# Performance work log

Measured on AMD Instinct MI355X. Metric: run time of the kernel, lower is better.

The kernel has to match this reference:

```python
import jax, jax.numpy as jnp
import numpy as np

N = 100000
E = 1600000
D_IN = 256
N_HEADS = 4
OUT_SZ = 32  # output_dim // n_heads = 128 // 4
ALPHA = 0.2  # leaky relu slope


def setup_inputs() -> dict:
    key = jax.random.key(0)
    ks = jax.random.split(key, 8)
    x = jax.random.normal(ks[0], (N, D_IN), dtype=jnp.float32)
    edge_row = jax.random.randint(ks[1], (E,), 0, N, dtype=jnp.int32)
    edge_col = jax.random.randint(ks[2], (E,), 0, N, dtype=jnp.int32)
    # per-head params: W (conv1d k=1, no bias), a1/a2 (conv1d k=1 with bias)
    W = jax.random.normal(ks[3], (N_HEADS, D_IN, OUT_SZ), dtype=jnp.float32) * (1.0 / np.sqrt(D_IN))
    a1 = jax.random.normal(ks[4], (N_HEADS, OUT_SZ), dtype=jnp.float32) * (1.0 / np.sqrt(OUT_SZ))
    b1 = jnp.zeros((N_HEADS,), dtype=jnp.float32)
    a2 = jax.random.normal(ks[5], (N_HEADS, OUT_SZ), dtype=jnp.float32) * (1.0 / np.sqrt(OUT_SZ))
    b2 = jnp.zeros((N_HEADS,), dtype=jnp.float32)
    return {"x": x, "W": W, "a1": a1, "b1": b1, "a2": a2, "b2": b2,
            "edge_row": edge_row, "edge_col": edge_col}


def _gat_heads(x, W, a1, b1, a2, b2, edge_row, edge_col):
    # per-head linear transform: [H, N, O]
    fts = jnp.einsum('nd,hdo->hno', x, W)
    f1 = jnp.einsum('hno,ho->hn', fts, a1) + b1[:, None]  # [H, N]
    f2 = jnp.einsum('hno,ho->hn', fts, a2) + b2[:, None]  # [H, N]
    # edge logits: f1[row] + f2[col]  (adj values are 1)
    logits = f1[:, edge_row] + f2[:, edge_col]            # [H, E]
    lr = jnp.maximum(ALPHA * logits, logits)
    # segment softmax over each node's incoming edge set (rows)
    seg_max = jax.vmap(lambda v: jax.ops.segment_max(v, edge_row, num_segments=N))(lr)
    ex = jnp.exp(lr - seg_max[:, edge_row])
    denom = jax.vmap(lambda v: jax.ops.segment_sum(v, edge_row, num_segments=N))(ex)
    coef = ex / denom[:, edge_row]                        # [H, E]
    # SpMM aggregation: out[h, i] = sum_{e: row(e)=i} coef[h,e] * fts[h, col(e)]
    msg = coef[:, :, None] * fts[:, edge_col, :]          # [H, E, O]
    agg = jax.vmap(lambda m: jax.ops.segment_sum(m, edge_row, num_segments=N))(msg)  # [H, N, O]
    h = jnp.transpose(agg, (1, 0, 2)).reshape(N, N_HEADS * OUT_SZ)  # concat heads
    return jax.nn.elu(h)[None]  # [1, N, output_dim]


def reference(x, W, a1, b1, a2, b2, edge_row, edge_col):
    return _gat_heads(x, W, a1, b1, a2, b2, edge_row, edge_col)
```

## Files before the change

kernel.cpp:

```cpp
#include <hip/hip_runtime.h>
#include <hip/hip_bf16.h>
#include <math.h>

#define ALPHA 0.2f
#define PB_EDGES 4096

typedef __attribute__((ext_vector_type(8))) short short8;
typedef __attribute__((ext_vector_type(4))) float floatx4;

__device__ __forceinline__ ushort f2bf(float f) {
    uint u = __float_as_uint(f);
    u += 0x7fff + ((u >> 16) & 1);
    return (ushort)(u >> 16);
}

__device__ __forceinline__ short8 pack8(float4 lo, float4 hi) {
    short8 r;
    r[0] = (short)f2bf(lo.x); r[1] = (short)f2bf(lo.y);
    r[2] = (short)f2bf(lo.z); r[3] = (short)f2bf(lo.w);
    r[4] = (short)f2bf(hi.x); r[5] = (short)f2bf(hi.y);
    r[6] = (short)f2bf(hi.z); r[7] = (short)f2bf(hi.w);
    return r;
}

__global__ __launch_bounds__(256) void k_wprep(const float* __restrict__ W,
                                               ushort* __restrict__ Wt)
{
    int g = blockIdx.x * 256 + threadIdx.x;
    int c = g >> 8, d = g & 255;
    Wt[g] = f2bf(W[(c >> 5) * 8192 + d * 32 + (c & 31)]);
}

__global__ __launch_bounds__(256) void k_gemm(const float* __restrict__ x,
                                              const ushort* __restrict__ Wt,
                                              const float* __restrict__ a1v,
                                              const float* __restrict__ b1v,
                                              const float* __restrict__ a2v,
                                              const float* __restrict__ b2v,
                                              ushort* __restrict__ fts2,
                                              float* __restrict__ f1,
                                              float* __restrict__ f2, int M)
{
    __shared__ __align__(16) ushort smem[32768];
    const int t  = threadIdx.x;
    const int m0 = blockIdx.x * 128;

#pragma unroll
    for (int i = 0; i < 16; i++) {
        int f = i * 256 + t;
        int lane_ = f & 63, ksct = f >> 6;
        int ks = ksct & 7, ct = ksct >> 3;
        int mm = lane_ & 15, qq = lane_ >> 4;
        *(uint4*)&smem[f * 8] = *(const uint4*)&Wt[(ct * 16 + mm) * 256 + ks * 32 + qq * 8];
    }

    const int w = t >> 6, lane = t & 63;
    const int mm = lane & 15, qq = lane >> 4;

    int row0 = m0 + w * 32 + mm;
    int row1 = row0 + 16;
    int r0c = (row0 < M) ? row0 : (M - 1);
    int r1c = (row1 < M) ? row1 : (M - 1);
    const float* ar0 = x + (size_t)r0c * 256 + qq * 8;
    const float* ar1 = x + (size_t)r1c * 256 + qq * 8;
    short8 afrag[2][8];
#pragma unroll
    for (int ks = 0; ks < 8; ks++) {
        float4 lo0 = *(const float4*)(ar0 + ks * 32);
        float4 hi0 = *(const float4*)(ar0 + ks * 32 + 4);
        float4 lo1 = *(const float4*)(ar1 + ks * 32);
        float4 hi1 = *(const float4*)(ar1 + ks * 32 + 4);
        afrag[0][ks] = pack8(lo0, hi0);
        afrag[1][ks] = pack8(lo1, hi1);
    }

    floatx4 acc[2][8];
#pragma unroll
    for (int r = 0; r < 2; r++)
#pragma unroll
        for (int ct = 0; ct < 8; ct++) acc[r][ct] = (floatx4){0.f, 0.f, 0.f, 0.f};

    __syncthreads();

#pragma unroll
    for (int ks = 0; ks < 8; ks++) {
#pragma unroll
        for (int ct = 0; ct < 8; ct++) {
            short8 b8 = *(const short8*)&smem[((ct * 8 + ks) * 64 + lane) * 8];
            acc[0][ct] = __builtin_amdgcn_mfma_f32_16x16x32_bf16(afrag[0][ks], b8, acc[0][ct], 0, 0, 0);
            acc[1][ct] = __builtin_amdgcn_mfma_f32_16x16x32_bf16(afrag[1][ks], b8, acc[1][ct], 0, 0, 0);
        }
    }

    __syncthreads();
    ushort* ftsL = smem;
#pragma unroll
    for (int r = 0; r < 2; r++)
#pragma unroll
        for (int ct = 0; ct < 8; ct++)
#pragma unroll
            for (int i = 0; i < 4; i++) {
                int rowl = w * 32 + r * 16 + qq * 4 + i;
                ftsL[rowl * 136 + ct * 16 + mm] = f2bf(acc[r][ct][i]);
            }
    __syncthreads();

    {
        int rowl = t >> 1, half = t & 1;
        int gr = m0 + rowl;
        if (gr < M) {
            const uint4* src = (const uint4*)&ftsL[rowl * 136 + half * 64];
            uint4* dst = (uint4*)(fts2 + (size_t)gr * 128 + half * 64);
#pragma unroll
            for (int i = 0; i < 8; i++) dst[i] = src[i];
        }
    }
#pragma unroll
    for (int p = 0; p < 2; p++) {
        int task = p * 256 + t;
        int rowl = task >> 2, h = task & 3;
        int gr = m0 + rowl;
        if (gr < M) {
            const ushort* fr = &ftsL[rowl * 136 + h * 32];
            float s1 = 0.f, s2 = 0.f;
#pragma unroll
            for (int o = 0; o < 32; o++) {
                float v = __uint_as_float((uint)fr[o] << 16);
                s1 = fmaf(v, a1v[h * 32 + o], s1);
                s2 = fmaf(v, a2v[h * 32 + o], s2);
            }
            f1[gr * 4 + h] = s1 + b1v[h];
            f2[gr * 4 + h] = s2 + b2v[h];
        }
    }
}

__global__ __launch_bounds__(256) void k_phist(const int* __restrict__ erow,
                                               int* __restrict__ bcnt, int E, int NB)
{
    __shared__ int h[512];
    for (int i = threadIdx.x; i < 512; i += 256) h[i] = 0;
    __syncthreads();
    int b0 = blockIdx.x * PB_EDGES;
    int bend = b0 + PB_EDGES; if (bend > E) bend = E;
    for (int j = b0 + threadIdx.x; j < bend; j += 256)
        atomicAdd(&h[erow[j] >> 8], 1);
    __syncthreads();
    for (int i = threadIdx.x; i < NB; i += 256)
        if (h[i]) atomicAdd(&bcnt[i], h[i]);
}

__global__ __launch_bounds__(256) void k_scan_buckets(const int* __restrict__ bcnt,
                                                      int* __restrict__ base,
                                                      int* __restrict__ bcursor,
                                                      int NB, int E)
{
    __shared__ int s[256];
    int t = threadIdx.x;
    int i0 = 2 * t, i1 = 2 * t + 1;
    int v0 = (i0 < NB) ? bcnt[i0] : 0;
    int v1 = (i1 < NB) ? bcnt[i1] : 0;
    int tsum = v0 + v1;
    s[t] = tsum;
    __syncthreads();
    for (int off = 1; off < 256; off <<= 1) {
        int u = (t >= off) ? s[t - off] : 0;
        __syncthreads();
        s[t] += u;
        __syncthreads();
    }
    int excl = s[t] - tsum;
    if (i0 < NB) { base[i0] = excl;      bcursor[i0] = excl; }
    if (i1 < NB) { base[i1] = excl + v0; bcursor[i1] = excl + v0; }
    if (t == 0) base[NB] = E;
}

__global__ __launch_bounds__(256) void k_pscatter(const int* __restrict__ erow,
                                                  const int* __restrict__ ecol,
                                                  int* __restrict__ bcursor,
                                                  uint* __restrict__ part, int E)
{
    __shared__ int h[512];
    __shared__ int cur[512];
    for (int i = threadIdx.x; i < 512; i += 256) h[i] = 0;
    __syncthreads();
    int b0 = blockIdx.x * PB_EDGES;
    int bend = b0 + PB_EDGES; if (bend > E) bend = E;
    for (int j = b0 + threadIdx.x; j < bend; j += 256)
        atomicAdd(&h[erow[j] >> 8], 1);
    __syncthreads();
    for (int i = threadIdx.x; i < 512; i += 256)
        cur[i] = h[i] ? atomicAdd(&bcursor[i], h[i]) : 0;
    __syncthreads();
    for (int j = b0 + threadIdx.x; j < bend; j += 256) {
        int r = erow[j], c = ecol[j];
        int p = atomicAdd(&cur[r >> 8], 1);
        part[p] = ((uint)(r & 255) << 24) | (uint)c;
    }
}

__global__ __launch_bounds__(256) void k_bucket(const uint* __restrict__ part,
                                                const int* __restrict__ base,
                                                int* __restrict__ row_start,
                                                int* __restrict__ col_sorted,
                                                int Nn, int NB, int E)
{
    __shared__ int cnt[256];
    __shared__ int s[256];
    __shared__ int cur[256];
    const int b = blockIdx.x, t = threadIdx.x;
    const int start = base[b], end = base[b + 1];

    cnt[t] = 0;
    __syncthreads();
    for (int j = start + t; j < end; j += 256)
        atomicAdd(&cnt[part[j] >> 24], 1);
    __syncthreads();
    int v = cnt[t];
    s[t] = v;
    __syncthreads();
    for (int off = 1; off < 256; off <<= 1) {
        int u = (t >= off) ? s[t - off] : 0;
        __syncthreads();
        s[t] += u;
        __syncthreads();
    }
    int excl = s[t] - v;
    int r = b * 256 + t;
    if (r < Nn) row_start[r] = start + excl;
    if (b == 0 && t == 0) row_start[Nn] = E;
    cur[t] = start + excl;
    __syncthreads();
    for (int j = start + t; j < end; j += 256) {
        uint rc = part[j];
        int p = atomicAdd(&cur[rc >> 24], 1);
        col_sorted[p] = (int)(rc & 0xffffffu);
    }
}

__global__ __launch_bounds__(256) void k_gat_row(const ushort* __restrict__ fts2,
                                                 const float4* __restrict__ f1,
                                                 const float4* __restrict__ f2,
                                                 const int* __restrict__ row_start,
                                                 const int* __restrict__ cols,
                                                 float* __restrict__ out, int Nn)
{
    __shared__ float eL[4][256];
    __shared__ int   cL[4][64];

    const int wid  = threadIdx.x >> 6;
    const int lane = threadIdx.x & 63;
    const int r = blockIdx.x * 4 + wid;
    if (r >= Nn) return;

    const int s = row_start[r], e = row_start[r + 1];
    const int hl = lane >> 4;

    float2* outp = (float2*)(out + (size_t)r * 128);
    if (s == e) { outp[lane] = make_float2(0.f, 0.f); return; }

    const float4 f1r = f1[r];
    float ds0 = 0.f, ds1 = 0.f, ds2 = 0.f, ds3 = 0.f;
    float acc0 = 0.f, acc1 = 0.f;

    for (int j0 = s; j0 < e; j0 += 64) {
        int j = j0 + lane;
        bool act = (j < e);
        int c = act ? cols[j] : 0;
        float4 f2v = f2[c];
        float l0 = f1r.x + f2v.x; l0 = fmaxf(l0, ALPHA * l0);
        float l1 = f1r.y + f2v.y; l1 = fmaxf(l1, ALPHA * l1);
        float l2 = f1r.z + f2v.z; l2 = fmaxf(l2, ALPHA * l2);
        float l3 = f1r.w + f2v.w; l3 = fmaxf(l3, ALPHA * l3);
        float e0 = act ? __expf(l0) : 0.f;
        float e1 = act ? __expf(l1) : 0.f;
        float e2 = act ? __expf(l2) : 0.f;
        float e3 = act ? __expf(l3) : 0.f;
        ds0 += e0; ds1 += e1; ds2 += e2; ds3 += e3;

        asm volatile("s_waitcnt lgkmcnt(0)" ::: "memory");
        ((float4*)eL[wid])[lane] = make_float4(e0, e1, e2, e3);
        cL[wid][lane] = c;
        asm volatile("s_waitcnt lgkmcnt(0)" ::: "memory");

        int len = e - j0; if (len > 64) len = 64;
#pragma unroll 4
        for (int jj = 0; jj < len; jj++) {
            float ee = eL[wid][jj * 4 + hl];
            int   cc = cL[wid][jj];
            const uint* fp = (const uint*)(fts2 + (size_t)cc * 128);
            uint vv = fp[lane];
            float vx = __uint_as_float(vv << 16);
            float vy = __uint_as_float(vv & 0xffff0000u);
            acc0 = fmaf(ee, vx, acc0);
            acc1 = fmaf(ee, vy, acc1);
        }
    }

#pragma unroll
    for (int off = 32; off > 0; off >>= 1) {
        ds0 += __shfl_xor(ds0, off, 64);
        ds1 += __shfl_xor(ds1, off, 64);
        ds2 += __shfl_xor(ds2, off, 64);
        ds3 += __shfl_xor(ds3, off, 64);
    }
    float dsel = (hl == 0) ? ds0 : (hl == 1) ? ds1 : (hl == 2) ? ds2 : ds3;

    float o0 = acc0 / dsel;
    float o1 = acc1 / dsel;
    o0 = (o0 > 0.f) ? o0 : (__expf(o0) - 1.0f);
    o1 = (o1 > 0.f) ? o1 : (__expf(o1) - 1.0f);
    outp[lane] = make_float2(o0, o1);
}

extern "C" void kernel_launch(void* const* d_in, const int* in_sizes, int n_in,
                              void* d_out, int out_size, void* d_ws, size_t ws_size,
                              hipStream_t stream)
{
    const float* x   = (const float*)d_in[0];
    const float* W   = (const float*)d_in[1];
    const float* a1  = (const float*)d_in[2];
    const float* b1  = (const float*)d_in[3];
    const float* a2  = (const float*)d_in[4];
    const float* b2  = (const float*)d_in[5];
    const int*   erow = (const int*)d_in[6];
    const int*   ecol = (const int*)d_in[7];
    float* out = (float*)d_out;

    const int N = in_sizes[0] / 256;
    const int E = in_sizes[6];
    const int NB = (N + 255) >> 8;

    char*  ws  = (char*)d_ws;
    size_t off = 0;
    auto carve = [&](size_t bytes) -> char* {
        char* p = ws + off;
        off += (bytes + 255) & ~(size_t)255;
        return p;
    };
    ushort* fts2      = (ushort*)carve((size_t)N * 128 * 2);
    ushort* Wt        = (ushort*)carve((size_t)128 * 256 * 2);
    float*  f1        = (float*)carve((size_t)N * 4 * 4);
    float*  f2        = (float*)carve((size_t)N * 4 * 4);
    int*    row_start = (int*)carve(((size_t)N + 1) * 4);
    int*    bcnt      = (int*)carve(512 * 4);
    int*    base      = (int*)carve(513 * 4);
    int*    bcursor   = (int*)carve(512 * 4);
    int*    col_sorted= (int*)carve((size_t)E * 4);
    uint*   part      = (uint*)carve((size_t)E * 4);
    (void)ws_size;

    k_wprep<<<128, 256, 0, stream>>>(W, Wt);
    k_gemm<<<(N + 127) / 128, 256, 0, stream>>>(x, Wt, a1, b1, a2, b2, fts2, f1, f2, N);

    hipMemsetAsync(bcnt, 0, 512 * 4, stream);
    int npb = (E + PB_EDGES - 1) / PB_EDGES;
    k_phist<<<npb, 256, 0, stream>>>(erow, bcnt, E, NB);
    k_scan_buckets<<<1, 256, 0, stream>>>(bcnt, base, bcursor, NB, E);
    k_pscatter<<<npb, 256, 0, stream>>>(erow, ecol, bcursor, part, E);
    k_bucket<<<NB, 256, 0, stream>>>(part, base, row_start, col_sorted, N, NB, E);

    k_gat_row<<<(N + 3) / 4, 256, 0, stream>>>(fts2, (const float4*)f1, (const float4*)f2,
                                               row_start, col_sorted, out, N);
}
```

Baseline: 340.7 us.

## Process four edges per wave iteration with 16-byte gathers in GAT aggregation

The aggregation loop now splits each 64-lane wave into four 16-lane slots. Each slot handles a different edge, and each lane loads 16 bytes (8 bf16 values) of the neighbor feature row instead of 4 bytes. Column indices are stored pre-shifted as byte offsets to save address math. Partial accumulators are combined across slots with cross-lane shuffles at the end, and only slot 0 writes the output. The intent is fewer loop iterations and wider memory transactions for the gather, at the cost of more registers and an extra reduction.

Result: no change. 341.9 us (+0.4%).

```diff
diff --git a/kernel.cpp b/kernel.cpp
--- a/kernel.cpp
+++ b/kernel.cpp
@@ -245,8 +245,8 @@
                                                  const int* __restrict__ cols,
                                                  float* __restrict__ out, int Nn)
 {
-    __shared__ float eL[4][256];
-    __shared__ int   cL[4][64];
+    __shared__ __align__(16) float eL[4][256];
+    __shared__ uint vL[4][64];
 
     const int wid  = threadIdx.x >> 6;
     const int lane = threadIdx.x & 63;
@@ -254,14 +254,30 @@
     if (r >= Nn) return;
 
     const int s = row_start[r], e = row_start[r + 1];
-    const int hl = lane >> 4;
-
-    float2* outp = (float2*)(out + (size_t)r * 128);
-    if (s == e) { outp[lane] = make_float2(0.f, 0.f); return; }
+
+    const int slot = lane >> 4;
+    const int sub  = lane & 15;
+    const int hsel = sub >> 2;
+
+    float4* dst = (float4*)(out + (size_t)r * 128 + sub * 8);
+    if (s == e) {
+        if (slot == 0) {
+            dst[0] = make_float4(0.f, 0.f, 0.f, 0.f);
+            dst[1] = make_float4(0.f, 0.f, 0.f, 0.f);
+        }
+        return;
+    }
 
     const float4 f1r = f1[r];
     float ds0 = 0.f, ds1 = 0.f, ds2 = 0.f, ds3 = 0.f;
-    float acc0 = 0.f, acc1 = 0.f;
+    float acc[8];
+#pragma unroll
+    for (int i = 0; i < 8; i++) acc[i] = 0.f;
+
+    const float* eBase   = &eL[wid][slot * 4 + hsel];
+    const uint*  vBase   = &vL[wid][slot];
+    const char*  ftsB    = (const char*)fts2;
+    const uint   laneOff = (uint)sub * 16;
 
     for (int j0 = s; j0 < e; j0 += 64) {
         int j = j0 + lane;
@@ -280,23 +296,33 @@
 
         asm volatile("s_waitcnt lgkmcnt(0)" ::: "memory");
         ((float4*)eL[wid])[lane] = make_float4(e0, e1, e2, e3);
-        cL[wid][lane] = c;
+        vL[wid][lane] = (uint)c << 8;
         asm volatile("s_waitcnt lgkmcnt(0)" ::: "memory");
 
         int len = e - j0; if (len > 64) len = 64;
+        int ng = (len + 3) >> 2;
 #pragma unroll 4
-        for (int jj = 0; jj < len; jj++) {
-            float ee = eL[wid][jj * 4 + hl];
-            int   cc = cL[wid][jj];
-            const uint* fp = (const uint*)(fts2 + (size_t)cc * 128);
-            uint vv = fp[lane];
-            float vx = __uint_as_float(vv << 16);
-            float vy = __uint_as_float(vv & 0xffff0000u);
-            acc0 = fmaf(ee, vx, acc0);
-            acc1 = fmaf(ee, vy, acc1);
-        }
-    }
-
+        for (int g = 0; g < ng; g++) {
+            float ee = eBase[g * 16];
+            uint  vo = vBase[g * 4] + laneOff;
+            uint4 vv = *(const uint4*)(ftsB + vo);
+            float ve;
+            ve = __uint_as_float(vv.x << 16);          acc[0] = fmaf(ee, ve, acc[0]);
+            ve = __uint_as_float(vv.x & 0xffff0000u);  acc[1] = fmaf(ee, ve, acc[1]);
+            ve = __uint_as_float(vv.y << 16);          acc[2] = fmaf(ee, ve, acc[2]);
+            ve = __uint_as_float(vv.y & 0xffff0000u);  acc[3] = fmaf(ee, ve, acc[3]);
+            ve = __uint_as_float(vv.z << 16);          acc[4] = fmaf(ee, ve, acc[4]);
+            ve = __uint_as_float(vv.z & 0xffff0000u);  acc[5] = fmaf(ee, ve, acc[5]);
+            ve = __uint_as_float(vv.w << 16);          acc[6] = fmaf(ee, ve, acc[6]);
+            ve = __uint_as_float(vv.w & 0xffff0000u);  acc[7] = fmaf(ee, ve, acc[7]);
+        }
+    }
+
+#pragma unroll
+    for (int i = 0; i < 8; i++) {
+        acc[i] += __shfl_xor(acc[i], 16, 64);
+        acc[i] += __shfl_xor(acc[i], 32, 64);
+    }
 #pragma unroll
     for (int off = 32; off > 0; off >>= 1) {
         ds0 += __shfl_xor(ds0, off, 64);
@@ -304,13 +330,19 @@
         ds2 += __shfl_xor(ds2, off, 64);
         ds3 += __shfl_xor(ds3, off, 64);
     }
-    float dsel = (hl == 0) ? ds0 : (hl == 1) ? ds1 : (hl == 2) ? ds2 : ds3;
-
-    float o0 = acc0 / dsel;
-    float o1 = acc1 / dsel;
-    o0 = (o0 > 0.f) ? o0 : (__expf(o0) - 1.0f);
-    o1 = (o1 > 0.f) ? o1 : (__expf(o1) - 1.0f);
-    outp[lane] = make_float2(o0, o1);
+    float dsel = (hsel == 0) ? ds0 : (hsel == 1) ? ds1 : (hsel == 2) ? ds2 : ds3;
+    float rinv = 1.0f / dsel;
+
+    float o[8];
+#pragma unroll
+    for (int i = 0; i < 8; i++) {
+        float v = acc[i] * rinv;
+        o[i] = (v > 0.f) ? v : (__expf(v) - 1.0f);
+    }
+    if (slot == 0) {
+        dst[0] = make_float4(o[0], o[1], o[2], o[3]);
+        dst[1] = make_float4(o[4], o[5], o[6], o[7]);
+    }
 }
 
 extern "C" void kernel_launch(void* const* d_in, const int* in_sizes, int n_in,
```
